# Optimization experiments

Hardware: AMD Instinct MI355X
Metric: run time of the kernel (lower is better)

Reference implementation:

```python
import jax, jax.numpy as jnp
import numpy as np

NUM_PATCH_X = 8   # P: patches per spatial axis
PATCH_EXTENT = 8  # pe: voxels per patch per axis
NF = 64           # feature channels


def setup_inputs() -> dict:
    key = jax.random.key(0)
    B = 4
    x = jax.random.normal(
        key, (B * NUM_PATCH_X ** 3, NF, PATCH_EXTENT, PATCH_EXTENT, PATCH_EXTENT),
        dtype=jnp.float32)
    return {"x": x}


def reference(x) -> jnp.ndarray:
    # Fold3D with stride == kernel_size is pure data movement:
    # out[b, c, p1*pe+e1, p2*pe+e2, p3*pe+e3] = x[b, p1, p2, p3, c, e1, e2, e3]
    P, pe, nf = NUM_PATCH_X, PATCH_EXTENT, NF
    B = x.shape[0] // (P ** 3)
    y = x.reshape(B, P, P, P, nf, pe, pe, pe)
    # -> (B, nf, P, pe, P, pe, P, pe): interleave patch-grid and intra-patch axes
    y = jnp.transpose(y, (0, 4, 1, 5, 2, 6, 3, 7))
    return y.reshape(B, nf, P * pe, P * pe, P * pe)
```

## Files before the change

### kernel.cpp

```cpp
#include <hip/hip_runtime.h>


__global__ __launch_bounds__(256) void fold3d_kernel(
    const float4* __restrict__ x, float4* __restrict__ out) {
    int bid = blockIdx.x;
    int c  = bid & 63;
    int t  = bid >> 6;
    int p2 = t & 7;  t >>= 3;
    int p1 = t & 7;
    int b  = t >> 3;

    const int inBaseBlk = (((b * 8 + p1) * 8 + p2) * 8) * 8192 + c * 128;
    const int outBaseBlk = ((b * 64 + c) * 64 + p1 * 8) * 64 * 16 + (p2 * 8) * 16;

    #pragma unroll
    for (int k = 0; k < 4; ++k) {
        int o = threadIdx.x + (k << 8);
        int e1 = o >> 7;
        int r  = o & 127;
        int e2 = r >> 4;
        int r2 = r & 15;
        int p3 = r2 >> 1;
        int h  = r2 & 1;

        int inIdx  = inBaseBlk + p3 * 8192 + (e1 * 8 + e2) * 2 + h;
        int outIdx = outBaseBlk + (e1 * 64 + e2) * 16 + p3 * 2 + h;

        out[outIdx] = x[inIdx];
    }
}

extern "C" void kernel_launch(void* const* d_in, const int* in_sizes, int n_in,
                              void* d_out, int out_size, void* d_ws, size_t ws_size,
                              hipStream_t stream) {
    const float4* x = (const float4*)d_in[0];
    float4* out = (float4*)d_out;
    dim3 grid(16384), block(256);
    fold3d_kernel<<<grid, block, 0, stream>>>(x, out);
}
```

Baseline: 426.9 us.

## Remap lanes for contiguous reads and writes via wavefront shuffles, nontemporal access

Reassigns each wave's lanes so that global loads cover 128-byte contiguous runs per p3 slice. Cross-lane shuffles then permute the data so each lane stores to consecutive output addresses, making stores fully contiguous per wave. Loads and stores use nontemporal builtins to avoid cache pollution in this streaming copy. The cost is four shuffles per float4 and an extra set of registers holding the loaded vectors.

```diff
diff --git a/kernel.cpp b/kernel.cpp
--- a/kernel.cpp
+++ b/kernel.cpp
@@ -1,8 +1,10 @@
 #include <hip/hip_runtime.h>
 
 
+typedef float v4f __attribute__((ext_vector_type(4)));
+
 __global__ __launch_bounds__(256) void fold3d_kernel(
-    const float4* __restrict__ x, float4* __restrict__ out) {
+    const v4f* __restrict__ x, v4f* __restrict__ out) {
     int bid = blockIdx.x;
     int c  = bid & 63;
     int t  = bid >> 6;
@@ -10,31 +12,43 @@
     int p1 = t & 7;
     int b  = t >> 3;
 
-    const int inBaseBlk = (((b * 8 + p1) * 8 + p2) * 8) * 8192 + c * 128;
-    const int outBaseBlk = ((b * 64 + c) * 64 + p1 * 8) * 64 * 16 + (p2 * 8) * 16;
+    const int inBase  = (((b * 8 + p1) * 8 + p2) * 8) * 8192 + c * 128;
+    const int outBase = ((b * 64 + c) * 64 + p1 * 8) * 1024 + p2 * 128;
+
+    const int lane = threadIdx.x & 63;
+    const int w    = threadIdx.x >> 6;
+
+    const int d   = lane;
+    const int src = (((d >> 1) & 7) << 3) + ((d >> 4) << 1) + (d & 1);
+
+    const int inLane = ((lane >> 3) << 13) + (lane & 7);
+
+    v4f v[4];
+    #pragma unroll
+    for (int k = 0; k < 4; ++k) {
+        int s = (w << 2) + k;
+        int inIdx = inBase + inLane + ((s >> 1) << 4) + ((s & 1) << 3);
+        v[k] = __builtin_nontemporal_load(&x[inIdx]);
+    }
 
     #pragma unroll
     for (int k = 0; k < 4; ++k) {
-        int o = threadIdx.x + (k << 8);
-        int e1 = o >> 7;
-        int r  = o & 127;
-        int e2 = r >> 4;
-        int r2 = r & 15;
-        int p3 = r2 >> 1;
-        int h  = r2 & 1;
-
-        int inIdx  = inBaseBlk + p3 * 8192 + (e1 * 8 + e2) * 2 + h;
-        int outIdx = outBaseBlk + (e1 * 64 + e2) * 16 + p3 * 2 + h;
-
-        out[outIdx] = x[inIdx];
+        int s = (w << 2) + k;
+        v4f g;
+        g.x = __shfl(v[k].x, src);
+        g.y = __shfl(v[k].y, src);
+        g.z = __shfl(v[k].z, src);
+        g.w = __shfl(v[k].w, src);
+        int outIdx = outBase + ((s >> 1) << 10) + ((s & 1) << 6) + d;
+        __builtin_nontemporal_store(g, &out[outIdx]);
     }
 }
 
 extern "C" void kernel_launch(void* const* d_in, const int* in_sizes, int n_in,
                               void* d_out, int out_size, void* d_ws, size_t ws_size,
                               hipStream_t stream) {
-    const float4* x = (const float4*)d_in[0];
-    float4* out = (float4*)d_out;
+    const v4f* x = (const v4f*)d_in[0];
+    v4f* out = (v4f*)d_out;
     dim3 grid(16384), block(256);
     fold3d_kernel<<<grid, block, 0, stream>>>(x, out);
 }
```

Result: faster. 414.9 us (-2.8%).
